# Optimization experiments

Measured on AMD Instinct MI355X. Metric: run time of the kernel, lower is better.

Reference implementation:

```python
import jax, jax.numpy as jnp
import numpy as np

B, S, D, O, H, E, K = 4, 1024, 1024, 1024, 2048, 16, 4


def setup_inputs() -> dict:
    key = jax.random.key(0)
    ks = jax.random.split(key, 8)
    x = jax.random.normal(ks[0], (B, S, D), dtype=jnp.float32)
    # gating params (unused by 'plain' gating math but present in the module)
    w_gate = jax.random.normal(ks[1], (D, E), dtype=jnp.float32) * 0.01
    w_noise = jnp.zeros((D, E), dtype=jnp.float32)
    # per-expert 2-layer MLP: Linear(D,H) + ReLU + Linear(H,O)
    W1 = jax.random.normal(ks[2], (E, D, H), dtype=jnp.float32) * (1.0 / np.sqrt(D))
    b1 = jnp.zeros((E, H), dtype=jnp.float32)
    W2 = jax.random.normal(ks[3], (E, H, O), dtype=jnp.float32) * (1.0 / np.sqrt(H))
    b2 = jnp.zeros((E, O), dtype=jnp.float32)
    return {"x": x, "w_gate": w_gate, "w_noise": w_noise,
            "W1": W1, "b1": b1, "W2": W2, "b2": b2}


def reference(x, w_gate, w_noise, W1, b1, W2, b2):
    # --- gating ('plain' policy): logits zeroed, expert 1 forced to 100 ---
    # (torch code computes x @ w_gate then overwrites with zeros_like, so
    #  w_gate/w_noise carry no gradient; gates are effectively constant.)
    logits = jnp.zeros((x.shape[0], x.shape[1], E), dtype=x.dtype).at[..., 1].set(100.0)
    top_vals, top_idx = jax.lax.top_k(logits, K)            # [B,S,K]
    gates_k = jax.nn.softmax(top_vals, axis=-1)             # softmax over top-k logits
    # dense gate matrix via scatter of top-k gates (one-hot combine)
    gates = jnp.einsum('bske,bsk->bse',
                       jax.nn.one_hot(top_idx, E, dtype=x.dtype), gates_k)  # [B,S,E]

    # --- per-expert FFN on all tokens, gated combine (zero gates kill
    #     contributions of non-selected experts, matching the torch loop) ---
    h = jax.nn.relu(jnp.einsum('bsd,edh->ebsh', x, W1) + b1[:, None, None, :])  # [E,B,S,H]
    y = jnp.einsum('ebsh,eho->ebso', h, W2) + b2[:, None, None, :]              # [E,B,S,O]
    out = jnp.einsum('ebso,bse->bso', y, gates)                                  # [B,S,O]
    return out
```

## Files before the change

kernel.cpp:

```cpp
#include <hip/hip_runtime.h>
#include <stdint.h>


typedef __bf16 bf16x8 __attribute__((ext_vector_type(8)));
typedef float f32x4 __attribute__((ext_vector_type(4)));

__device__ __forceinline__ unsigned short f2bf(float f) {
  uint32_t u = __builtin_bit_cast(uint32_t, f);
  u += 0x7fffu + ((u >> 16) & 1u);
  return (unsigned short)(u >> 16);
}

__global__ void k_convert(const float* __restrict__ in, unsigned short* __restrict__ out, int n) {
  int i = (blockIdx.x * blockDim.x + threadIdx.x) * 4;
  if (i >= n) return;
  float4 v = *(const float4*)(in + i);
  ushort4 o;
  o.x = f2bf(v.x); o.y = f2bf(v.y); o.z = f2bf(v.z); o.w = f2bf(v.w);
  *(ushort4*)(out + i) = o;
}

__global__ void k_transpose(const float* __restrict__ in, unsigned short* __restrict__ out,
                            int R, int C) {
  __shared__ float t[32][33];
  const int tx = threadIdx.x, ty = threadIdx.y;
  const int c0 = blockIdx.x * 32, r0 = blockIdx.y * 32;
#pragma unroll
  for (int k = 0; k < 4; ++k) {
    int r = r0 + ty + k * 8;
    t[ty + k * 8][tx] = in[(size_t)r * C + c0 + tx];
  }
  __syncthreads();
#pragma unroll
  for (int k = 0; k < 4; ++k) {
    int p = c0 + ty + k * 8;
    out[(size_t)p * R + r0 + tx] = f2bf(t[tx][ty + k * 8]);
  }
}

__device__ __forceinline__ void glds16(const unsigned short* g, unsigned short* l) {
  __builtin_amdgcn_global_load_lds(
      (const __attribute__((address_space(1))) unsigned int*)g,
      (__attribute__((address_space(3))) unsigned int*)l, 16, 0, 0);
}

template <bool BF16OUT_RELU>
__global__ __launch_bounds__(256) void k_gemm(const unsigned short* __restrict__ A,
                                              const unsigned short* __restrict__ Bt,
                                              const float* __restrict__ bias,
                                              void* __restrict__ Cout,
                                              int Nn, int Kk) {
  __shared__ unsigned short As[128 * 32];
  __shared__ unsigned short Bs[128 * 32];

  const int tid = threadIdx.x;
  const int wave = tid >> 6, lane = tid & 63;
  const int wm = (wave >> 1) * 64, wn = (wave & 1) * 64;
  const int m0 = blockIdx.y * 128, n0 = blockIdx.x * 128;
  const int q = lane >> 4, l16 = lane & 15;

  f32x4 acc[4][4] = {};

  const int c1 = tid, c2 = tid + 256;
  const unsigned short* gA1 = A + (size_t)(m0 + (c1 >> 2)) * Kk + (c1 & 3) * 8;
  const unsigned short* gA2 = A + (size_t)(m0 + (c2 >> 2)) * Kk + (c2 & 3) * 8;
  const unsigned short* gB1 = Bt + (size_t)(n0 + (c1 >> 2)) * Kk + (c1 & 3) * 8;
  const unsigned short* gB2 = Bt + (size_t)(n0 + (c2 >> 2)) * Kk + (c2 & 3) * 8;
  unsigned short* lA1 = As + c1 * 8;
  unsigned short* lA2 = As + c2 * 8;
  unsigned short* lB1 = Bs + c1 * 8;
  unsigned short* lB2 = Bs + c2 * 8;

  for (int k0 = 0; k0 < Kk; k0 += 32) {
    __syncthreads();
    glds16(gA1 + k0, lA1);
    glds16(gA2 + k0, lA2);
    glds16(gB1 + k0, lB1);
    glds16(gB2 + k0, lB2);
    __syncthreads();

    bf16x8 af[4], bfr[4];
#pragma unroll
    for (int i = 0; i < 4; ++i)
      af[i] = *(const bf16x8*)&As[(wm + i * 16 + l16) * 32 + q * 8];
#pragma unroll
    for (int j = 0; j < 4; ++j)
      bfr[j] = *(const bf16x8*)&Bs[(wn + j * 16 + l16) * 32 + q * 8];
#pragma unroll
    for (int i = 0; i < 4; ++i)
#pragma unroll
      for (int j = 0; j < 4; ++j)
        acc[i][j] = __builtin_amdgcn_mfma_f32_16x16x32_bf16(af[i], bfr[j], acc[i][j], 0, 0, 0);
  }

  float bv[4];
#pragma unroll
  for (int j = 0; j < 4; ++j) bv[j] = bias[n0 + wn + j * 16 + l16];

#pragma unroll
  for (int i = 0; i < 4; ++i) {
    const int row_base = m0 + wm + i * 16 + q * 4;
#pragma unroll
    for (int j = 0; j < 4; ++j) {
      const int col = n0 + wn + j * 16 + l16;
#pragma unroll
      for (int r = 0; r < 4; ++r) {
        float v = acc[i][j][r] + bv[j];
        if (BF16OUT_RELU) {
          v = fmaxf(v, 0.0f);
          ((unsigned short*)Cout)[(size_t)(row_base + r) * Nn + col] = f2bf(v);
        } else {
          ((float*)Cout)[(size_t)(row_base + r) * Nn + col] = v;
        }
      }
    }
  }
}

extern "C" void kernel_launch(void* const* d_in, const int* in_sizes, int n_in,
                              void* d_out, int out_size, void* d_ws, size_t ws_size,
                              hipStream_t stream) {
  const float* x  = (const float*)d_in[0];
  const float* W1 = (const float*)d_in[3];
  const float* b1 = (const float*)d_in[4];
  const float* W2 = (const float*)d_in[5];
  const float* b2 = (const float*)d_in[6];

  const int M = 4096, D = 1024, H = 2048, O = 1024;

  char* ws = (char*)d_ws;
  unsigned short* Xbf = (unsigned short*)(ws);
  unsigned short* W1t = (unsigned short*)(ws + (8u << 20));
  unsigned short* W2t = (unsigned short*)(ws + (12u << 20));
  unsigned short* H1  = (unsigned short*)(ws + (16u << 20));

  const float* W1e = W1 + (size_t)1 * D * H;
  const float* W2e = W2 + (size_t)1 * H * O;
  const float* b1e = b1 + H;
  const float* b2e = b2 + O;

  k_convert<<<(M * D / 4 + 255) / 256, 256, 0, stream>>>(x, Xbf, M * D);
  k_transpose<<<dim3(H / 32, D / 32), dim3(32, 8), 0, stream>>>(W1e, W1t, D, H);
  k_transpose<<<dim3(O / 32, H / 32), dim3(32, 8), 0, stream>>>(W2e, W2t, H, O);

  k_gemm<true><<<dim3(H / 128, M / 128), 256, 0, stream>>>(Xbf, W1t, b1e, H1, H, D);
  k_gemm<false><<<dim3(O / 128, M / 128), 256, 0, stream>>>(H1, W2t, b2e, d_out, O, H);
}
```

Baseline: 314.4 us.

## Double-buffer GEMM LDS tiles and merge prep kernels into one launch

The GEMM k-loop now uses two LDS buffers for the A and B tiles. The next K-slice is prefetched with global_load_lds while MFMAs run on the current slice, which drops one barrier per iteration and hides global load latency. The convert kernel and the two transpose kernels are merged into a single block-indexed k_prep launch to cut launch overhead. The cost is twice the LDS per block, which may lower occupancy, and correctness now depends on the barrier waiting for the async LDS loads.

```diff
diff --git a/kernel.cpp b/kernel.cpp
--- a/kernel.cpp
+++ b/kernel.cpp
@@ -11,31 +11,35 @@
   return (unsigned short)(u >> 16);
 }
 
-__global__ void k_convert(const float* __restrict__ in, unsigned short* __restrict__ out, int n) {
-  int i = (blockIdx.x * blockDim.x + threadIdx.x) * 4;
-  if (i >= n) return;
-  float4 v = *(const float4*)(in + i);
-  ushort4 o;
-  o.x = f2bf(v.x); o.y = f2bf(v.y); o.z = f2bf(v.z); o.w = f2bf(v.w);
-  *(ushort4*)(out + i) = o;
-}
-
-__global__ void k_transpose(const float* __restrict__ in, unsigned short* __restrict__ out,
-                            int R, int C) {
+__global__ __launch_bounds__(256) void k_prep(const float* __restrict__ x,
+                                              const float* __restrict__ W1e,
+                                              const float* __restrict__ W2e,
+                                              unsigned short* __restrict__ Xbf,
+                                              unsigned short* __restrict__ W1t,
+                                              unsigned short* __restrict__ W2t) {
+  const int b = blockIdx.x;
+  const int tid = threadIdx.x;
+  if (b < 4096) {
+    int i = (b * 256 + tid) * 4;
+    float4 v = *(const float4*)(x + i);
+    ushort4 o;
+    o.x = f2bf(v.x); o.y = f2bf(v.y); o.z = f2bf(v.z); o.w = f2bf(v.w);
+    *(ushort4*)(Xbf + i) = o;
+    return;
+  }
   __shared__ float t[32][33];
-  const int tx = threadIdx.x, ty = threadIdx.y;
-  const int c0 = blockIdx.x * 32, r0 = blockIdx.y * 32;
+  const float* in; unsigned short* out; int R, C, bx, by;
+  if (b < 6144) { int tb = b - 4096; in = W1e; out = W1t; R = 1024; C = 2048; bx = tb & 63; by = tb >> 6; }
+  else          { int tb = b - 6144; in = W2e; out = W2t; R = 2048; C = 1024; bx = tb & 31; by = tb >> 5; }
+  const int tx = tid & 31, ty = tid >> 5;
+  const int c0 = bx * 32, r0 = by * 32;
 #pragma unroll
-  for (int k = 0; k < 4; ++k) {
-    int r = r0 + ty + k * 8;
-    t[ty + k * 8][tx] = in[(size_t)r * C + c0 + tx];
-  }
+  for (int k = 0; k < 4; ++k)
+    t[ty + k * 8][tx] = in[(size_t)(r0 + ty + k * 8) * C + c0 + tx];
   __syncthreads();
 #pragma unroll
-  for (int k = 0; k < 4; ++k) {
-    int p = c0 + ty + k * 8;
-    out[(size_t)p * R + r0 + tx] = f2bf(t[tx][ty + k * 8]);
-  }
+  for (int k = 0; k < 4; ++k)
+    out[(size_t)(c0 + ty + k * 8) * R + r0 + tx] = f2bf(t[tx][ty + k * 8]);
 }
 
 __device__ __forceinline__ void glds16(const unsigned short* g, unsigned short* l) {
@@ -50,8 +54,8 @@
                                               const float* __restrict__ bias,
                                               void* __restrict__ Cout,
                                               int Nn, int Kk) {
-  __shared__ unsigned short As[128 * 32];
-  __shared__ unsigned short Bs[128 * 32];
+  __shared__ unsigned short As[2][128 * 32];
+  __shared__ unsigned short Bs[2][128 * 32];
 
   const int tid = threadIdx.x;
   const int wave = tid >> 6, lane = tid & 63;
@@ -66,26 +70,34 @@
   const unsigned short* gA2 = A + (size_t)(m0 + (c2 >> 2)) * Kk + (c2 & 3) * 8;
   const unsigned short* gB1 = Bt + (size_t)(n0 + (c1 >> 2)) * Kk + (c1 & 3) * 8;
   const unsigned short* gB2 = Bt + (size_t)(n0 + (c2 >> 2)) * Kk + (c2 & 3) * 8;
-  unsigned short* lA1 = As + c1 * 8;
-  unsigned short* lA2 = As + c2 * 8;
-  unsigned short* lB1 = Bs + c1 * 8;
-  unsigned short* lB2 = Bs + c2 * 8;
+  const int o1 = c1 * 8, o2 = c2 * 8;
 
-  for (int k0 = 0; k0 < Kk; k0 += 32) {
+  glds16(gA1, &As[0][o1]);
+  glds16(gA2, &As[0][o2]);
+  glds16(gB1, &Bs[0][o1]);
+  glds16(gB2, &Bs[0][o2]);
+
+  const int ktot = Kk >> 5;
+  for (int kt = 0; kt < ktot; ++kt) {
+    const int cur = kt & 1;
     __syncthreads();
-    glds16(gA1 + k0, lA1);
-    glds16(gA2 + k0, lA2);
-    glds16(gB1 + k0, lB1);
-    glds16(gB2 + k0, lB2);
-    __syncthreads();
+
+    if (kt + 1 < ktot) {
+      const int nxt = cur ^ 1;
+      const int k0 = (kt + 1) << 5;
+      glds16(gA1 + k0, &As[nxt][o1]);
+      glds16(gA2 + k0, &As[nxt][o2]);
+      glds16(gB1 + k0, &Bs[nxt][o1]);
+      glds16(gB2 + k0, &Bs[nxt][o2]);
+    }
 
     bf16x8 af[4], bfr[4];
 #pragma unroll
     for (int i = 0; i < 4; ++i)
-      af[i] = *(const bf16x8*)&As[(wm + i * 16 + l16) * 32 + q * 8];
+      af[i] = *(const bf16x8*)&As[cur][(wm + i * 16 + l16) * 32 + q * 8];
 #pragma unroll
     for (int j = 0; j < 4; ++j)
-      bfr[j] = *(const bf16x8*)&Bs[(wn + j * 16 + l16) * 32 + q * 8];
+      bfr[j] = *(const bf16x8*)&Bs[cur][(wn + j * 16 + l16) * 32 + q * 8];
 #pragma unroll
     for (int i = 0; i < 4; ++i)
 #pragma unroll
@@ -139,9 +151,7 @@
   const float* b1e = b1 + H;
   const float* b2e = b2 + O;
 
-  k_convert<<<(M * D / 4 + 255) / 256, 256, 0, stream>>>(x, Xbf, M * D);
-  k_transpose<<<dim3(H / 32, D / 32), dim3(32, 8), 0, stream>>>(W1e, W1t, D, H);
-  k_transpose<<<dim3(O / 32, H / 32), dim3(32, 8), 0, stream>>>(W2e, W2t, H, O);
+  k_prep<<<8192, 256, 0, stream>>>(x, W1e, W2e, Xbf, W1t, W2t);
 
   k_gemm<true><<<dim3(H / 128, M / 128), 256, 0, stream>>>(Xbf, W1t, b1e, H1, H, D);
   k_gemm<false><<<dim3(O / 128, M / 128), 256, 0, stream>>>(H1, W2t, b2e, d_out, O, H);
```

After: 306.7 us. 2.5% less time.
